# Performance work log

Measured on AMD Instinct MI355X. Metric: run time of the kernel, lower is better.

The kernel has to match this reference:

```python
import jax, jax.numpy as jnp
import numpy as np

TEMP = 0.07
EPS = 1e-12  # matches torch F.normalize default eps


def _l2norm(x):
    n = jnp.sqrt(jnp.sum(x * x, axis=-1, keepdims=True))
    return x / jnp.maximum(n, EPS)


def setup_inputs() -> dict:
    key = jax.random.key(0)
    kq, kk = jax.random.split(key)
    N, D = 16384, 256
    q = jax.random.normal(kq, (N, D), dtype=jnp.float32)
    k = jax.random.normal(kk, (N, D), dtype=jnp.float32)
    return {"q": q, "k": k}


def reference(q, k):
    qn = _l2norm(q)
    kn = _l2norm(k)
    logits = (qn @ kn.T) / TEMP            # [N, N]
    # cross-entropy with labels = arange(N): mean over rows of (logsumexp - diag)
    lse = jax.nn.logsumexp(logits, axis=-1)  # [N]
    diag = jnp.diagonal(logits)              # [N]
    return jnp.mean(lse - diag)
```

## Files before the change

kernel.cpp:

```cpp
#include <hip/hip_runtime.h>
#include <hip/hip_bf16.h>
#include <cstdint>
#include <cstddef>

#define NROWS 16384
#define DDIM  256
#define SPLITS 16
#define NTILES 256

typedef __attribute__((ext_vector_type(4))) float f32x4;
typedef __attribute__((ext_vector_type(4))) float fl4;
typedef __attribute__((ext_vector_type(4))) int   i32x4;
typedef __attribute__((ext_vector_type(8))) int   i32x8;

constexpr float SCALE_EXP2 = 20.609929155556627f;
constexpr float LN2F       = 0.69314718055994531f;
constexpr float INV_T      = 14.285714285714286f;

__device__ inline void gload_lds16(const void* g, void* l) {
  __builtin_amdgcn_global_load_lds(
      (const __attribute__((address_space(1))) void*)g,
      (__attribute__((address_space(3))) void*)l, 16, 0, 0);
}

__global__ __launch_bounds__(256) void norm_kernel(
    const float* __restrict__ q, const float* __restrict__ k,
    unsigned char* __restrict__ qn, unsigned char* __restrict__ kn,
    float* __restrict__ diag, float* __restrict__ rowsum,
    float* __restrict__ out)
{
  const int wave = threadIdx.x >> 6, lane = threadIdx.x & 63;
  const int row = blockIdx.x * 4 + wave;
  const size_t off = (size_t)row * DDIM + lane * 4;

  fl4 vq = *(const fl4*)(q + off);
  fl4 vk = *(const fl4*)(k + off);
  float ssq = vq.x * vq.x + vq.y * vq.y + vq.z * vq.z + vq.w * vq.w;
  float ssk = vk.x * vk.x + vk.y * vk.y + vk.z * vk.z + vk.w * vk.w;
  float dot = vq.x * vk.x + vq.y * vk.y + vq.z * vk.z + vq.w * vk.w;
#pragma unroll
  for (int m = 1; m < 64; m <<= 1) {
    ssq += __shfl_xor(ssq, m, 64);
    ssk += __shfl_xor(ssk, m, 64);
    dot += __shfl_xor(dot, m, 64);
  }
  float rq = 1.0f / fmaxf(sqrtf(ssq), 1e-12f);
  float rk = 1.0f / fmaxf(sqrtf(ssk), 1e-12f);

  float sq = rq * SCALE_EXP2;
  int pq = __builtin_amdgcn_cvt_pk_fp8_f32(vq.x * sq, vq.y * sq, 0, false);
  pq     = __builtin_amdgcn_cvt_pk_fp8_f32(vq.z * sq, vq.w * sq, pq, true);
  *(int*)(qn + off) = pq;
  int pk = __builtin_amdgcn_cvt_pk_fp8_f32(vk.x * rk, vk.y * rk, 0, false);
  pk     = __builtin_amdgcn_cvt_pk_fp8_f32(vk.z * rk, vk.w * rk, pk, true);
  *(int*)(kn + off) = pk;

  if (lane == 0) {
    diag[row]   = dot * rq * rk * INV_T;
    rowsum[row] = 0.0f;
    if (row == 0) out[0] = 0.0f;
  }
}

__global__ __launch_bounds__(256) void lse_kernel(
    const unsigned char* __restrict__ qn, const unsigned char* __restrict__ kn,
    float* __restrict__ rowsum)
{
  __shared__ __attribute__((aligned(16))) unsigned char Bs[64 * DDIM];

  const int tid  = threadIdx.x;
  const int wave = tid >> 6, lane = tid & 63;
  const int l15  = lane & 15, quad = lane >> 4;
  const int split = blockIdx.x % SPLITS;
  const int rb    = blockIdx.x / SPLITS;
  const int wrow  = rb * 256 + wave * 64;
  const int t0 = (split * NTILES) / SPLITS;
  const int t1 = ((split + 1) * NTILES) / SPLITS;

  i32x8 A[4][2];
#pragma unroll
  for (int s = 0; s < 4; ++s) {
    const unsigned char* ap = qn + (size_t)(wrow + s * 16 + l15) * DDIM + quad * 32;
#pragma unroll
    for (int ks = 0; ks < 2; ++ks)
      A[s][ks] = *(const i32x8*)(ap + ks * 128);
  }

  float sums[4][4];
#pragma unroll
  for (int s = 0; s < 4; ++s)
#pragma unroll
    for (int r = 0; r < 4; ++r) sums[s][r] = 0.0f;

  for (int ct = t0; ct < t1; ++ct) {
    const unsigned char* kbase = kn + (size_t)ct * 64 * DDIM;
    __syncthreads();
#pragma unroll
    for (int i = 0; i < 4; ++i) {
      int L = i * 256 + tid;
      int n = L >> 4, jj = L & 15;
      int j = jj ^ (n & 15);
      gload_lds16(kbase + (size_t)n * DDIM + j * 16, (void*)(Bs + L * 16));
    }
    __syncthreads();

#pragma unroll
    for (int cs = 0; cs < 4; ++cs) {
      int n  = cs * 16 + l15;
      int nb = n & 15;
      const unsigned char* brow = Bs + n * DDIM;
      f32x4 acc0 = {0.f, 0.f, 0.f, 0.f};
      f32x4 acc1 = {0.f, 0.f, 0.f, 0.f};
      f32x4 acc2 = {0.f, 0.f, 0.f, 0.f};
      f32x4 acc3 = {0.f, 0.f, 0.f, 0.f};
#pragma unroll
      for (int ks = 0; ks < 2; ++ks) {
        int c0 = ks * 8 + quad * 2;
        i32x4 lo = *(const i32x4*)(brow + ((c0 ^ nb) * 16));
        i32x4 hi = *(const i32x4*)(brow + (((c0 + 1) ^ nb) * 16));
        i32x8 b = {lo.x, lo.y, lo.z, lo.w, hi.x, hi.y, hi.z, hi.w};
        acc0 = __builtin_amdgcn_mfma_scale_f32_16x16x128_f8f6f4(A[0][ks], b, acc0, 0, 0, 0, 127, 0, 127);
        acc1 = __builtin_amdgcn_mfma_scale_f32_16x16x128_f8f6f4(A[1][ks], b, acc1, 0, 0, 0, 127, 0, 127);
        acc2 = __builtin_amdgcn_mfma_scale_f32_16x16x128_f8f6f4(A[2][ks], b, acc2, 0, 0, 0, 127, 0, 127);
        acc3 = __builtin_amdgcn_mfma_scale_f32_16x16x128_f8f6f4(A[3][ks], b, acc3, 0, 0, 0, 127, 0, 127);
      }
#pragma unroll
      for (int r = 0; r < 4; ++r) {
        sums[0][r] += __builtin_amdgcn_exp2f(acc0[r]);
        sums[1][r] += __builtin_amdgcn_exp2f(acc1[r]);
        sums[2][r] += __builtin_amdgcn_exp2f(acc2[r]);
        sums[3][r] += __builtin_amdgcn_exp2f(acc3[r]);
      }
    }
  }

#pragma unroll
  for (int s = 0; s < 4; ++s)
#pragma unroll
    for (int r = 0; r < 4; ++r) {
      float v = sums[s][r];
      v += __shfl_xor(v, 1, 64);
      v += __shfl_xor(v, 2, 64);
      v += __shfl_xor(v, 4, 64);
      v += __shfl_xor(v, 8, 64);
      if (l15 == 0) atomicAdd(&rowsum[wrow + s * 16 + quad * 4 + r], v);
    }
}

__global__ void final_kernel(const float* __restrict__ rowsum,
                             const float* __restrict__ diag,
                             float* __restrict__ out)
{
  int row = blockIdx.x * 256 + threadIdx.x;
  float c = __builtin_amdgcn_logf(rowsum[row]) * LN2F - diag[row];
#pragma unroll
  for (int m = 1; m < 64; m <<= 1) c += __shfl_xor(c, m, 64);
  __shared__ float red[4];
  int wave = threadIdx.x >> 6, lane = threadIdx.x & 63;
  if (lane == 0) red[wave] = c;
  __syncthreads();
  if (threadIdx.x == 0) {
    float s = red[0] + red[1] + red[2] + red[3];
    atomicAdd(out, s * (1.0f / NROWS));
  }
}

extern "C" void kernel_launch(void* const* d_in, const int* in_sizes, int n_in,
                              void* d_out, int out_size, void* d_ws, size_t ws_size,
                              hipStream_t stream)
{
  const float* q = (const float*)d_in[0];
  const float* k = (const float*)d_in[1];
  float* out = (float*)d_out;

  char* ws = (char*)d_ws;
  unsigned char* qn = (unsigned char*)ws;
  unsigned char* kn = (unsigned char*)(ws + (4u << 20));
  float* diag   = (float*)(ws + (8u << 20));
  float* rowsum = (float*)(ws + (8u << 20) + (64u << 10));

  norm_kernel <<<NROWS / 4, 256, 0, stream>>>(q, k, qn, kn, diag, rowsum, out);
  lse_kernel  <<<(NROWS / 256) * SPLITS, 256, 0, stream>>>(qn, kn, rowsum);
  final_kernel<<<NROWS / 256, 256, 0, stream>>>(rowsum, diag, out);
}
```

Before: 148.3 us.

## Load K tiles directly from global memory into registers, dropping LDS staging

The LSE kernel no longer stages each 64-row K tile into swizzled shared memory with global_load_lds and two barriers per tile. Each wave now reads its B fragments straight from global memory (through L1/L2) into registers and feeds them to the MFMAs. This removes the barriers and LDS traffic. In exchange the four waves of a block each fetch the same K data separately, so cache bandwidth use rises, and there is no explicit prefetch to hide global load latency.

```diff
diff --git a/kernel.cpp b/kernel.cpp
--- a/kernel.cpp
+++ b/kernel.cpp
@@ -10,18 +10,11 @@
 
 typedef __attribute__((ext_vector_type(4))) float f32x4;
 typedef __attribute__((ext_vector_type(4))) float fl4;
-typedef __attribute__((ext_vector_type(4))) int   i32x4;
 typedef __attribute__((ext_vector_type(8))) int   i32x8;
 
 constexpr float SCALE_EXP2 = 20.609929155556627f;
 constexpr float LN2F       = 0.69314718055994531f;
 constexpr float INV_T      = 14.285714285714286f;
-
-__device__ inline void gload_lds16(const void* g, void* l) {
-  __builtin_amdgcn_global_load_lds(
-      (const __attribute__((address_space(1))) void*)g,
-      (__attribute__((address_space(3))) void*)l, 16, 0, 0);
-}
 
 __global__ __launch_bounds__(256) void norm_kernel(
     const float* __restrict__ q, const float* __restrict__ k,
@@ -66,14 +59,12 @@
     const unsigned char* __restrict__ qn, const unsigned char* __restrict__ kn,
     float* __restrict__ rowsum)
 {
-  __shared__ __attribute__((aligned(16))) unsigned char Bs[64 * DDIM];
-
   const int tid  = threadIdx.x;
-  const int wave = tid >> 6, lane = tid & 63;
+  const int lane = tid & 63;
   const int l15  = lane & 15, quad = lane >> 4;
   const int split = blockIdx.x % SPLITS;
   const int rb    = blockIdx.x / SPLITS;
-  const int wrow  = rb * 256 + wave * 64;
+  const int wrow  = rb * 256 + (tid >> 6) * 64;
   const int t0 = (split * NTILES) / SPLITS;
   const int t1 = ((split + 1) * NTILES) / SPLITS;
 
@@ -92,38 +83,26 @@
 #pragma unroll
     for (int r = 0; r < 4; ++r) sums[s][r] = 0.0f;
 
-  for (int ct = t0; ct < t1; ++ct) {
-    const unsigned char* kbase = kn + (size_t)ct * 64 * DDIM;
-    __syncthreads();
-#pragma unroll
-    for (int i = 0; i < 4; ++i) {
-      int L = i * 256 + tid;
-      int n = L >> 4, jj = L & 15;
-      int j = jj ^ (n & 15);
-      gload_lds16(kbase + (size_t)n * DDIM + j * 16, (void*)(Bs + L * 16));
-    }
-    __syncthreads();
+  const unsigned char* kb = kn + (size_t)t0 * 64 * DDIM + (size_t)l15 * DDIM + quad * 32;
 
+  for (int ct = t0; ct < t1; ++ct, kb += 64 * DDIM) {
 #pragma unroll
     for (int cs = 0; cs < 4; ++cs) {
-      int n  = cs * 16 + l15;
-      int nb = n & 15;
-      const unsigned char* brow = Bs + n * DDIM;
+      const unsigned char* bp = kb + cs * 16 * DDIM;
+      i32x8 b0 = *(const i32x8*)(bp);
+      i32x8 b1 = *(const i32x8*)(bp + 128);
       f32x4 acc0 = {0.f, 0.f, 0.f, 0.f};
       f32x4 acc1 = {0.f, 0.f, 0.f, 0.f};
       f32x4 acc2 = {0.f, 0.f, 0.f, 0.f};
       f32x4 acc3 = {0.f, 0.f, 0.f, 0.f};
-#pragma unroll
-      for (int ks = 0; ks < 2; ++ks) {
-        int c0 = ks * 8 + quad * 2;
-        i32x4 lo = *(const i32x4*)(brow + ((c0 ^ nb) * 16));
-        i32x4 hi = *(const i32x4*)(brow + (((c0 + 1) ^ nb) * 16));
-        i32x8 b = {lo.x, lo.y, lo.z, lo.w, hi.x, hi.y, hi.z, hi.w};
-        acc0 = __builtin_amdgcn_mfma_scale_f32_16x16x128_f8f6f4(A[0][ks], b, acc0, 0, 0, 0, 127, 0, 127);
-        acc1 = __builtin_amdgcn_mfma_scale_f32_16x16x128_f8f6f4(A[1][ks], b, acc1, 0, 0, 0, 127, 0, 127);
-        acc2 = __builtin_amdgcn_mfma_scale_f32_16x16x128_f8f6f4(A[2][ks], b, acc2, 0, 0, 0, 127, 0, 127);
-        acc3 = __builtin_amdgcn_mfma_scale_f32_16x16x128_f8f6f4(A[3][ks], b, acc3, 0, 0, 0, 127, 0, 127);
-      }
+      acc0 = __builtin_amdgcn_mfma_scale_f32_16x16x128_f8f6f4(A[0][0], b0, acc0, 0, 0, 0, 127, 0, 127);
+      acc1 = __builtin_amdgcn_mfma_scale_f32_16x16x128_f8f6f4(A[1][0], b0, acc1, 0, 0, 0, 127, 0, 127);
+      acc2 = __builtin_amdgcn_mfma_scale_f32_16x16x128_f8f6f4(A[2][0], b0, acc2, 0, 0, 0, 127, 0, 127);
+      acc3 = __builtin_amdgcn_mfma_scale_f32_16x16x128_f8f6f4(A[3][0], b0, acc3, 0, 0, 0, 127, 0, 127);
+      acc0 = __builtin_amdgcn_mfma_scale_f32_16x16x128_f8f6f4(A[0][1], b1, acc0, 0, 0, 0, 127, 0, 127);
+      acc1 = __builtin_amdgcn_mfma_scale_f32_16x16x128_f8f6f4(A[1][1], b1, acc1, 0, 0, 0, 127, 0, 127);
+      acc2 = __builtin_amdgcn_mfma_scale_f32_16x16x128_f8f6f4(A[2][1], b1, acc2, 0, 0, 0, 127, 0, 127);
+      acc3 = __builtin_amdgcn_mfma_scale_f32_16x16x128_f8f6f4(A[3][1], b1, acc3, 0, 0, 0, 127, 0, 127);
 #pragma unroll
       for (int r = 0; r < 4; ++r) {
         sums[0][r] += __builtin_amdgcn_exp2f(acc0[r]);
```

Result: slower. 202.1 us (+36.3%).

## Per-wave double-buffered K staging with vmcnt waits instead of block barriers

Applied to the files above, without the earlier changes.

Each wave now stages its own 16-column K tiles into a private double-buffered LDS region using direct global-to-LDS loads. It waits with s_waitcnt vmcnt rather than __syncthreads, so the loads of the next tile overlap with the MFMA and exp2 work on the current one. The aim is to remove block-wide barrier stalls and exposed load latency. In exchange, each wave loads all K columns itself, so the four waves no longer share tiles and per-block LDS and L2 traffic rises fourfold. Correctness also depends on hand-counted vmcnt values and on per-lane LDS-write visibility without a barrier.

```diff
diff --git a/kernel.cpp b/kernel.cpp
--- a/kernel.cpp
+++ b/kernel.cpp
@@ -6,7 +6,7 @@
 #define NROWS 16384
 #define DDIM  256
 #define SPLITS 16
-#define NTILES 256
+#define TPS   64
 
 typedef __attribute__((ext_vector_type(4))) float f32x4;
 typedef __attribute__((ext_vector_type(4))) float fl4;
@@ -66,7 +66,7 @@
     const unsigned char* __restrict__ qn, const unsigned char* __restrict__ kn,
     float* __restrict__ rowsum)
 {
-  __shared__ __attribute__((aligned(16))) unsigned char Bs[64 * DDIM];
+  __shared__ __attribute__((aligned(16))) unsigned char Bs[32768];
 
   const int tid  = threadIdx.x;
   const int wave = tid >> 6, lane = tid & 63;
@@ -74,8 +74,24 @@
   const int split = blockIdx.x % SPLITS;
   const int rb    = blockIdx.x / SPLITS;
   const int wrow  = rb * 256 + wave * 64;
-  const int t0 = (split * NTILES) / SPLITS;
-  const int t1 = ((split + 1) * NTILES) / SPLITS;
+  const int col_base = split * (TPS * 16);
+
+  unsigned char* wb = Bs + wave * 8192;
+
+  auto stage = [&](int ct, int buf) {
+    const unsigned char* kbase = kn + (size_t)(col_base + ct * 16) * DDIM;
+    unsigned char* dst = wb + buf * 4096 + lane * 16;
+#pragma unroll
+    for (int i = 0; i < 4; ++i) {
+      const int n = i * 4 + quad;
+      gload_lds16(kbase + (size_t)n * DDIM + ((l15 ^ n) * 16), dst + i * 1024);
+    }
+  };
+
+  const int o00 = ((quad * 2    ) ^ l15) * 16;
+  const int o01 = ((quad * 2 + 1) ^ l15) * 16;
+  const int o10 = ((quad * 2 + 8) ^ l15) * 16;
+  const int o11 = ((quad * 2 + 9) ^ l15) * 16;
 
   i32x8 A[4][2];
 #pragma unroll
@@ -92,46 +108,46 @@
 #pragma unroll
     for (int r = 0; r < 4; ++r) sums[s][r] = 0.0f;
 
-  for (int ct = t0; ct < t1; ++ct) {
-    const unsigned char* kbase = kn + (size_t)ct * 64 * DDIM;
-    __syncthreads();
-#pragma unroll
-    for (int i = 0; i < 4; ++i) {
-      int L = i * 256 + tid;
-      int n = L >> 4, jj = L & 15;
-      int j = jj ^ (n & 15);
-      gload_lds16(kbase + (size_t)n * DDIM + j * 16, (void*)(Bs + L * 16));
-    }
-    __syncthreads();
-
-#pragma unroll
-    for (int cs = 0; cs < 4; ++cs) {
-      int n  = cs * 16 + l15;
-      int nb = n & 15;
-      const unsigned char* brow = Bs + n * DDIM;
-      f32x4 acc0 = {0.f, 0.f, 0.f, 0.f};
-      f32x4 acc1 = {0.f, 0.f, 0.f, 0.f};
-      f32x4 acc2 = {0.f, 0.f, 0.f, 0.f};
-      f32x4 acc3 = {0.f, 0.f, 0.f, 0.f};
-#pragma unroll
-      for (int ks = 0; ks < 2; ++ks) {
-        int c0 = ks * 8 + quad * 2;
-        i32x4 lo = *(const i32x4*)(brow + ((c0 ^ nb) * 16));
-        i32x4 hi = *(const i32x4*)(brow + (((c0 + 1) ^ nb) * 16));
-        i32x8 b = {lo.x, lo.y, lo.z, lo.w, hi.x, hi.y, hi.z, hi.w};
-        acc0 = __builtin_amdgcn_mfma_scale_f32_16x16x128_f8f6f4(A[0][ks], b, acc0, 0, 0, 0, 127, 0, 127);
-        acc1 = __builtin_amdgcn_mfma_scale_f32_16x16x128_f8f6f4(A[1][ks], b, acc1, 0, 0, 0, 127, 0, 127);
-        acc2 = __builtin_amdgcn_mfma_scale_f32_16x16x128_f8f6f4(A[2][ks], b, acc2, 0, 0, 0, 127, 0, 127);
-        acc3 = __builtin_amdgcn_mfma_scale_f32_16x16x128_f8f6f4(A[3][ks], b, acc3, 0, 0, 0, 127, 0, 127);
-      }
-#pragma unroll
-      for (int r = 0; r < 4; ++r) {
-        sums[0][r] += __builtin_amdgcn_exp2f(acc0[r]);
-        sums[1][r] += __builtin_amdgcn_exp2f(acc1[r]);
-        sums[2][r] += __builtin_amdgcn_exp2f(acc2[r]);
-        sums[3][r] += __builtin_amdgcn_exp2f(acc3[r]);
-      }
-    }
+  stage(0, 0);
+  stage(1, 1);
+
+  for (int ct = 0; ct < TPS; ++ct) {
+    const int cur = ct & 1;
+    if (ct + 1 < TPS) { asm volatile("s_waitcnt vmcnt(4)" ::: "memory"); }
+    else              { asm volatile("s_waitcnt vmcnt(0)" ::: "memory"); }
+
+    const unsigned char* brow = wb + cur * 4096 + l15 * 256;
+    f32x4 acc0 = {0.f, 0.f, 0.f, 0.f};
+    f32x4 acc1 = {0.f, 0.f, 0.f, 0.f};
+    f32x4 acc2 = {0.f, 0.f, 0.f, 0.f};
+    f32x4 acc3 = {0.f, 0.f, 0.f, 0.f};
+    {
+      i32x4 lo = *(const i32x4*)(brow + o00);
+      i32x4 hi = *(const i32x4*)(brow + o01);
+      i32x8 b = {lo.x, lo.y, lo.z, lo.w, hi.x, hi.y, hi.z, hi.w};
+      acc0 = __builtin_amdgcn_mfma_scale_f32_16x16x128_f8f6f4(A[0][0], b, acc0, 0, 0, 0, 127, 0, 127);
+      acc1 = __builtin_amdgcn_mfma_scale_f32_16x16x128_f8f6f4(A[1][0], b, acc1, 0, 0, 0, 127, 0, 127);
+      acc2 = __builtin_amdgcn_mfma_scale_f32_16x16x128_f8f6f4(A[2][0], b, acc2, 0, 0, 0, 127, 0, 127);
+      acc3 = __builtin_amdgcn_mfma_scale_f32_16x16x128_f8f6f4(A[3][0], b, acc3, 0, 0, 0, 127, 0, 127);
+    }
+    {
+      i32x4 lo = *(const i32x4*)(brow + o10);
+      i32x4 hi = *(const i32x4*)(brow + o11);
+      i32x8 b = {lo.x, lo.y, lo.z, lo.w, hi.x, hi.y, hi.z, hi.w};
+      acc0 = __builtin_amdgcn_mfma_scale_f32_16x16x128_f8f6f4(A[0][1], b, acc0, 0, 0, 0, 127, 0, 127);
+      acc1 = __builtin_amdgcn_mfma_scale_f32_16x16x128_f8f6f4(A[1][1], b, acc1, 0, 0, 0, 127, 0, 127);
+      acc2 = __builtin_amdgcn_mfma_scale_f32_16x16x128_f8f6f4(A[2][1], b, acc2, 0, 0, 0, 127, 0, 127);
+      acc3 = __builtin_amdgcn_mfma_scale_f32_16x16x128_f8f6f4(A[3][1], b, acc3, 0, 0, 0, 127, 0, 127);
+    }
+#pragma unroll
+    for (int r = 0; r < 4; ++r) {
+      sums[0][r] += __builtin_amdgcn_exp2f(acc0[r]);
+      sums[1][r] += __builtin_amdgcn_exp2f(acc1[r]);
+      sums[2][r] += __builtin_amdgcn_exp2f(acc2[r]);
+      sums[3][r] += __builtin_amdgcn_exp2f(acc3[r]);
+    }
+
+    if (ct + 2 < TPS) stage(ct + 2, cur);
   }
 
 #pragma unroll
```

Result: no change. 147.1 us (-0.8%).
